# Kernel optimization log

Hardware: AMD Instinct MI355X
Metric: run time of the kernel (lower is better)

## Reference

```python
import jax, jax.numpy as jnp
import numpy as np

B, N, H = 4, 256, 256
BN_EPS = 1e-5
ETA_EPS = 1e-20


def setup_inputs() -> dict:
    key = jax.random.key(0)
    k1, k2, k3, k4 = jax.random.split(key, 4)
    scale = 1.0 / np.sqrt(H)
    return {
        "nodes_features": jax.random.normal(k1, (B, N, H), dtype=jnp.float32),
        "edges_features": jax.random.normal(k2, (B, N, N, H), dtype=jnp.float32),
        "W1": jax.random.normal(k3, (H, H), dtype=jnp.float32) * scale,
        "W2": jax.random.normal(k4, (H, H), dtype=jnp.float32) * scale,
        "gamma": jnp.ones((H,), dtype=jnp.float32),
        "beta": jnp.zeros((H,), dtype=jnp.float32),
    }


def reference(nodes_features, edges_features, W1, W2, gamma, beta):
    # Linear projections (nn.Linear: y = x @ W.T, no bias)
    x_left = jnp.einsum('bnh,oh->bno', nodes_features, W1)       # (B,N,H)
    x_w2 = jnp.einsum('bnh,oh->bno', nodes_features, W2)         # (B,N,H)

    # Edge gating: sigmoid-normalize over neighbor axis j (dim=2)
    sig = jax.nn.sigmoid(edges_features)                         # (B,N,N,H)
    eta = sig / (jnp.sum(sig, axis=2, keepdims=True) + ETA_EPS)  # (B,N,N,H)

    # Weighted aggregation: sum_j eta[b,i,j,h] * x_w2[b,j,h]
    right = jnp.einsum('bijh,bjh->bih', eta, x_w2)               # (B,N,H)

    equ = x_left + right                                         # (B,N,H)

    # BatchNorm1d over channel H with batch stats over (B, N) (training mode,
    # track_running_stats=False -> always uses batch statistics, biased var)
    mean = jnp.mean(equ, axis=(0, 1))                            # (H,)
    var = jnp.var(equ, axis=(0, 1))                              # (H,) biased
    normed = (equ - mean) * jax.lax.rsqrt(var + BN_EPS)
    return normed * gamma + beta
```

## Files before the change

### kernel.cpp

```cpp
#include <hip/hip_runtime.h>
#include <cstddef>

#define BB 4
#define NN 256
#define HH 256
#define BN_EPS 1e-5f
#define ETA_EPS 1e-20f

typedef float f4 __attribute__((ext_vector_type(4)));

__device__ __forceinline__ float fast_sigmoid(float x) {
    float ex = __expf(-x);
    return __builtin_amdgcn_rcpf(1.f + ex);
}

__global__ __launch_bounds__(256) void transpose_kernel(
    const float* __restrict__ W1, const float* __restrict__ W2,
    float* __restrict__ WT1, float* __restrict__ WT2)
{
    const int which = blockIdx.x >> 4;
    const int tile  = blockIdx.x & 15;
    const int tr = (tile >> 2) << 6, tc = (tile & 3) << 6;
    const float* __restrict__ W  = which ? W2 : W1;
    float* __restrict__ WT       = which ? WT2 : WT1;

    __shared__ float tl[64][65];
    const int c = threadIdx.x & 63, p0 = threadIdx.x >> 6;
#pragma unroll
    for (int p = 0; p < 16; ++p) {
        int r = p * 4 + p0;
        tl[c][r] = W[(tr + r) * HH + tc + c];
    }
    __syncthreads();
#pragma unroll
    for (int p = 0; p < 16; ++p) {
        int cc = p * 4 + p0;
        WT[(tc + cc) * HH + tr + c] = tl[cc][c];
    }
}

__global__ __launch_bounds__(256) void proj_kernel(
    const float* __restrict__ nodes, const float* __restrict__ WT1,
    const float* __restrict__ WT2, float* __restrict__ xleft,
    float* __restrict__ xw2)
{
    const int which = blockIdx.x >> 7;
    const int rb    = blockIdx.x & 127;
    const float* __restrict__ WT = which ? WT2 : WT1;
    float* __restrict__ out      = which ? xw2 : xleft;
    const int t = threadIdx.x;

    __shared__ float xs[8][HH];
    {
        f4* xs4 = reinterpret_cast<f4*>(xs);
        const f4* nodes4 = reinterpret_cast<const f4*>(nodes) + rb * 512;
#pragma unroll
        for (int m = 0; m < 2; ++m) xs4[m * 256 + t] = nodes4[m * 256 + t];
    }
    __syncthreads();

    const int oq = t & 63;
    const int hg = t >> 6;
    const f4* __restrict__ WT4 = reinterpret_cast<const f4*>(WT);

    f4 acc[8];
#pragma unroll
    for (int r = 0; r < 8; ++r) acc[r] = (f4){0.f, 0.f, 0.f, 0.f};

    for (int hh = 0; hh < 64; ++hh) {
        const int h = hg * 64 + hh;
        f4 wv = WT4[h * 64 + oq];
#pragma unroll
        for (int r = 0; r < 8; ++r)
            acc[r] += xs[r][h] * wv;
    }

    __shared__ f4 ps[4][8][64];
#pragma unroll
    for (int r = 0; r < 8; ++r) ps[hg][r][oq] = acc[r];
    __syncthreads();

#pragma unroll
    for (int m = 0; m < 2; ++m) {
        int idx = m * 256 + t;
        int r = idx >> 6, o = idx & 63;
        f4 v = ps[0][r][o] + ps[1][r][o] + ps[2][r][o] + ps[3][r][o];
        reinterpret_cast<f4*>(out)[(rb * 8 + r) * 64 + o] = v;
    }
}

__global__ __launch_bounds__(1024) void edge_kernel(
    const float* __restrict__ edges, const float* __restrict__ xw2,
    const float* __restrict__ xleft, float* __restrict__ equ)
{
    const int blk = blockIdx.x;
    const int ig  = blk >> 2;
    const int hs4 = (blk & 3) * 16;
    const int bi0 = ig * 8;
    const int b   = bi0 >> 8;
    const int t   = threadIdx.x;

    __shared__ f4 xw_s[NN][16];

    const f4* __restrict__ xw4 =
        reinterpret_cast<const f4*>(xw2) + (size_t)b * NN * 64;
#pragma unroll
    for (int m = 0; m < 4; ++m) {
        int idx = m * 1024 + t;
        int j = idx >> 4, q = idx & 15;
        xw_s[j][q] = xw4[j * 64 + hs4 + q];
    }
    __syncthreads();

    const int q  = t & 15;
    const int jl = (t >> 4) & 3;
    const int w  = t >> 6;
    const int il = w & 7;
    const int jh = w >> 3;

    const f4* __restrict__ erow =
        reinterpret_cast<const f4*>(edges) +
        ((size_t)(bi0 + il) * NN + jh * 128 + jl) * 64 + hs4 + q;

    float s0[4] = {0.f, 0.f, 0.f, 0.f};
    float s1[4] = {0.f, 0.f, 0.f, 0.f};

#pragma unroll 4
    for (int jj = 0; jj < 32; ++jj) {
        f4 e  = __builtin_nontemporal_load(erow + jj * 256);
        f4 xw = xw_s[jh * 128 + jj * 4 + jl][q];
#pragma unroll
        for (int k = 0; k < 4; ++k) {
            float sg = fast_sigmoid(e[k]);
            s0[k] += sg;
            s1[k] += sg * xw[k];
        }
    }
    __syncthreads();

    float* red = reinterpret_cast<float*>(xw_s);
    {
        const int g = jh * 4 + jl;
        f4* r0 = reinterpret_cast<f4*>(red) + (g * 8 + il) * 16 + q;
        f4* r1 = r0 + 1024;
        *r0 = (f4){s0[0], s0[1], s0[2], s0[3]};
        *r1 = (f4){s1[0], s1[1], s1[2], s1[3]};
    }
    __syncthreads();

    if (t < 512) {
        const int il2 = t >> 6;
        const int ch  = t & 63;
        float S0 = 0.f, S1 = 0.f;
#pragma unroll
        for (int g = 0; g < 8; ++g) {
            S0 += red[(g * 8 + il2) * 64 + ch];
            S1 += red[(g * 8 + il2) * 64 + ch + 4096];
        }
        const size_t off = (size_t)(bi0 + il2) * HH + hs4 * 4 + ch;
        equ[off] = xleft[off] + S1 / (S0 + ETA_EPS);
    }
}

__global__ __launch_bounds__(1024) void stats_kernel(
    const float* __restrict__ equ, const float* __restrict__ gamma,
    const float* __restrict__ beta, float* __restrict__ scale,
    float* __restrict__ shift)
{
    const int t     = threadIdx.x;
    const int ql    = t & 3;
    const int rg    = t >> 2;
    const int qbase = blockIdx.x * 4;

    const f4* __restrict__ equ4 = reinterpret_cast<const f4*>(equ);

    float s[4] = {0.f, 0.f, 0.f, 0.f};
    float qq[4] = {0.f, 0.f, 0.f, 0.f};
    for (int r = rg; r < BB * NN; r += 256) {
        f4 v = equ4[r * 64 + qbase + ql];
#pragma unroll
        for (int k = 0; k < 4; ++k) { s[k] += v[k]; qq[k] += v[k] * v[k]; }
    }

    __shared__ float sp[256][17];
    __shared__ float qp[256][17];
    __shared__ float sp2[16][17];
    __shared__ float qp2[16][17];
#pragma unroll
    for (int k = 0; k < 4; ++k) { sp[rg][ql * 4 + k] = s[k]; qp[rg][ql * 4 + k] = qq[k]; }
    __syncthreads();

    if (t < 256) {
        const int ch = t & 15, seg = t >> 4;
        float S = 0.f, Q = 0.f;
#pragma unroll
        for (int g = 0; g < 16; ++g) { S += sp[seg * 16 + g][ch]; Q += qp[seg * 16 + g][ch]; }
        sp2[seg][ch] = S; qp2[seg][ch] = Q;
    }
    __syncthreads();

    if (t < 16) {
        float S = 0.f, Q = 0.f;
#pragma unroll
        for (int g = 0; g < 16; ++g) { S += sp2[g][t]; Q += qp2[g][t]; }
        const float inv_n = 1.f / (float)(BB * NN);
        float mean = S * inv_n;
        float var  = Q * inv_n - mean * mean;
        float rstd = rsqrtf(var + BN_EPS);
        int cc = blockIdx.x * 16 + t;
        float g  = gamma[cc];
        float bt = beta[cc];
        scale[cc] = rstd * g;
        shift[cc] = bt - mean * rstd * g;
    }
}

__global__ __launch_bounds__(256) void norm_kernel(
    const float* __restrict__ equ, const float* __restrict__ scale,
    const float* __restrict__ shift, float* __restrict__ out)
{
    const int idx = blockIdx.x * 256 + threadIdx.x;
    f4 e  = reinterpret_cast<const f4*>(equ)[idx];
    const int c4 = idx & 63;
    f4 sc = reinterpret_cast<const f4*>(scale)[c4];
    f4 sh = reinterpret_cast<const f4*>(shift)[c4];
    f4 o;
#pragma unroll
    for (int k = 0; k < 4; ++k) o[k] = e[k] * sc[k] + sh[k];
    reinterpret_cast<f4*>(out)[idx] = o;
}

extern "C" void kernel_launch(void* const* d_in, const int* in_sizes, int n_in,
                              void* d_out, int out_size, void* d_ws, size_t ws_size,
                              hipStream_t stream) {
    (void)in_sizes; (void)n_in; (void)out_size; (void)ws_size;

    const float* nodes = (const float*)d_in[0];
    const float* edges = (const float*)d_in[1];
    const float* W1    = (const float*)d_in[2];
    const float* W2    = (const float*)d_in[3];
    const float* gamma = (const float*)d_in[4];
    const float* beta  = (const float*)d_in[5];
    float* out = (float*)d_out;

    const int nBN_H = BB * NN * HH;
    float* ws    = (float*)d_ws;
    float* xleft = ws;
    float* xw2   = ws + nBN_H;
    float* equ   = ws + 2 * nBN_H;
    float* scale = ws + 3 * nBN_H;
    float* shift = ws + 3 * nBN_H + 256;
    float* WT1   = ws + 3 * nBN_H + 512;
    float* WT2   = WT1 + HH * HH;

    transpose_kernel<<<32, 256, 0, stream>>>(W1, W2, WT1, WT2);
    proj_kernel<<<256, 256, 0, stream>>>(nodes, WT1, WT2, xleft, xw2);
    edge_kernel<<<512, 1024, 0, stream>>>(edges, xw2, xleft, equ);
    stats_kernel<<<16, 1024, 0, stream>>>(equ, gamma, beta, scale, shift);
    norm_kernel<<<256, 256, 0, stream>>>(equ, scale, shift, out);
}
```

Baseline: 71.37 us.

## Restructure edge kernel to one row per block and fuse stats with norm

```diff
diff --git a/kernel.cpp b/kernel.cpp
--- a/kernel.cpp
+++ b/kernel.cpp
@@ -89,46 +89,28 @@
     }
 }
 
-__global__ __launch_bounds__(1024) void edge_kernel(
+__global__ __launch_bounds__(512, 6) void edge_kernel(
     const float* __restrict__ edges, const float* __restrict__ xw2,
     const float* __restrict__ xleft, float* __restrict__ equ)
 {
-    const int blk = blockIdx.x;
-    const int ig  = blk >> 2;
-    const int hs4 = (blk & 3) * 16;
-    const int bi0 = ig * 8;
-    const int b   = bi0 >> 8;
-    const int t   = threadIdx.x;
-
-    __shared__ f4 xw_s[NN][16];
-
+    const int bi = blockIdx.x;
+    const int b  = bi >> 8;
+    const int t  = threadIdx.x;
+    const int q  = t & 63;
+    const int jg = t >> 6;
+
+    const f4* __restrict__ e4 =
+        reinterpret_cast<const f4*>(edges) + ((size_t)bi * NN + jg * 32) * 64 + q;
     const f4* __restrict__ xw4 =
-        reinterpret_cast<const f4*>(xw2) + (size_t)b * NN * 64;
-#pragma unroll
-    for (int m = 0; m < 4; ++m) {
-        int idx = m * 1024 + t;
-        int j = idx >> 4, q = idx & 15;
-        xw_s[j][q] = xw4[j * 64 + hs4 + q];
-    }
-    __syncthreads();
-
-    const int q  = t & 15;
-    const int jl = (t >> 4) & 3;
-    const int w  = t >> 6;
-    const int il = w & 7;
-    const int jh = w >> 3;
-
-    const f4* __restrict__ erow =
-        reinterpret_cast<const f4*>(edges) +
-        ((size_t)(bi0 + il) * NN + jh * 128 + jl) * 64 + hs4 + q;
-
-    float s0[4] = {0.f, 0.f, 0.f, 0.f};
-    float s1[4] = {0.f, 0.f, 0.f, 0.f};
-
-#pragma unroll 4
+        reinterpret_cast<const f4*>(xw2) + ((size_t)b * NN + jg * 32) * 64 + q;
+
+    f4 s0 = (f4){0.f, 0.f, 0.f, 0.f};
+    f4 s1 = (f4){0.f, 0.f, 0.f, 0.f};
+
+#pragma unroll 2
     for (int jj = 0; jj < 32; ++jj) {
-        f4 e  = __builtin_nontemporal_load(erow + jj * 256);
-        f4 xw = xw_s[jh * 128 + jj * 4 + jl][q];
+        f4 e  = __builtin_nontemporal_load(e4 + (size_t)jj * 64);
+        f4 xw = xw4[(size_t)jj * 64];
 #pragma unroll
         for (int k = 0; k < 4; ++k) {
             float sg = fast_sigmoid(e[k]);
@@ -136,98 +118,78 @@
             s1[k] += sg * xw[k];
         }
     }
-    __syncthreads();
-
-    float* red = reinterpret_cast<float*>(xw_s);
-    {
-        const int g = jh * 4 + jl;
-        f4* r0 = reinterpret_cast<f4*>(red) + (g * 8 + il) * 16 + q;
-        f4* r1 = r0 + 1024;
-        *r0 = (f4){s0[0], s0[1], s0[2], s0[3]};
-        *r1 = (f4){s1[0], s1[1], s1[2], s1[3]};
-    }
-    __syncthreads();
-
-    if (t < 512) {
-        const int il2 = t >> 6;
-        const int ch  = t & 63;
-        float S0 = 0.f, S1 = 0.f;
-#pragma unroll
-        for (int g = 0; g < 8; ++g) {
-            S0 += red[(g * 8 + il2) * 64 + ch];
-            S1 += red[(g * 8 + il2) * 64 + ch + 4096];
+
+    __shared__ f4 red0[8][64];
+    __shared__ f4 red1[8][64];
+    red0[jg][q] = s0;
+    red1[jg][q] = s1;
+    __syncthreads();
+
+    if (t < 64) {
+        f4 S0 = (f4){0.f, 0.f, 0.f, 0.f};
+        f4 S1 = (f4){0.f, 0.f, 0.f, 0.f};
+#pragma unroll
+        for (int g = 0; g < 8; ++g) { S0 += red0[g][t]; S1 += red1[g][t]; }
+        f4 xl = reinterpret_cast<const f4*>(xleft)[bi * 64 + t];
+        f4 o;
+#pragma unroll
+        for (int k = 0; k < 4; ++k) o[k] = xl[k] + S1[k] / (S0[k] + ETA_EPS);
+        reinterpret_cast<f4*>(equ)[bi * 64 + t] = o;
+    }
+}
+
+__global__ __launch_bounds__(1024) void statsnorm_kernel(
+    const float* __restrict__ equ, const float* __restrict__ gamma,
+    const float* __restrict__ beta, float* __restrict__ out)
+{
+    const int cq = blockIdx.x;
+    const int t  = threadIdx.x;
+    const int lane = t & 63, w = t >> 6;
+
+    f4 v = reinterpret_cast<const f4*>(equ)[t * 64 + cq];
+    f4 s = v;
+    f4 qs = v * v;
+
+#pragma unroll
+    for (int off = 32; off >= 1; off >>= 1) {
+#pragma unroll
+        for (int k = 0; k < 4; ++k) {
+            s[k]  += __shfl_xor(s[k], off);
+            qs[k] += __shfl_xor(qs[k], off);
         }
-        const size_t off = (size_t)(bi0 + il2) * HH + hs4 * 4 + ch;
-        equ[off] = xleft[off] + S1 / (S0 + ETA_EPS);
-    }
-}
-
-__global__ __launch_bounds__(1024) void stats_kernel(
-    const float* __restrict__ equ, const float* __restrict__ gamma,
-    const float* __restrict__ beta, float* __restrict__ scale,
-    float* __restrict__ shift)
-{
-    const int t     = threadIdx.x;
-    const int ql    = t & 3;
-    const int rg    = t >> 2;
-    const int qbase = blockIdx.x * 4;
-
-    const f4* __restrict__ equ4 = reinterpret_cast<const f4*>(equ);
-
-    float s[4] = {0.f, 0.f, 0.f, 0.f};
-    float qq[4] = {0.f, 0.f, 0.f, 0.f};
-    for (int r = rg; r < BB * NN; r += 256) {
-        f4 v = equ4[r * 64 + qbase + ql];
-#pragma unroll
-        for (int k = 0; k < 4; ++k) { s[k] += v[k]; qq[k] += v[k] * v[k]; }
-    }
-
-    __shared__ float sp[256][17];
-    __shared__ float qp[256][17];
-    __shared__ float sp2[16][17];
-    __shared__ float qp2[16][17];
-#pragma unroll
-    for (int k = 0; k < 4; ++k) { sp[rg][ql * 4 + k] = s[k]; qp[rg][ql * 4 + k] = qq[k]; }
-    __syncthreads();
-
-    if (t < 256) {
-        const int ch = t & 15, seg = t >> 4;
-        float S = 0.f, Q = 0.f;
-#pragma unroll
-        for (int g = 0; g < 16; ++g) { S += sp[seg * 16 + g][ch]; Q += qp[seg * 16 + g][ch]; }
-        sp2[seg][ch] = S; qp2[seg][ch] = Q;
-    }
-    __syncthreads();
-
-    if (t < 16) {
-        float S = 0.f, Q = 0.f;
-#pragma unroll
-        for (int g = 0; g < 16; ++g) { S += sp2[g][t]; Q += qp2[g][t]; }
+    }
+
+    __shared__ f4 ws_[16][2];
+    if (lane == 0) { ws_[w][0] = s; ws_[w][1] = qs; }
+    __syncthreads();
+
+    __shared__ f4 sc_s, sh_s;
+    if (t == 0) {
+        f4 S = (f4){0.f, 0.f, 0.f, 0.f};
+        f4 Q = (f4){0.f, 0.f, 0.f, 0.f};
+#pragma unroll
+        for (int g = 0; g < 16; ++g) { S += ws_[g][0]; Q += ws_[g][1]; }
         const float inv_n = 1.f / (float)(BB * NN);
-        float mean = S * inv_n;
-        float var  = Q * inv_n - mean * mean;
-        float rstd = rsqrtf(var + BN_EPS);
-        int cc = blockIdx.x * 16 + t;
-        float g  = gamma[cc];
-        float bt = beta[cc];
-        scale[cc] = rstd * g;
-        shift[cc] = bt - mean * rstd * g;
-    }
-}
-
-__global__ __launch_bounds__(256) void norm_kernel(
-    const float* __restrict__ equ, const float* __restrict__ scale,
-    const float* __restrict__ shift, float* __restrict__ out)
-{
-    const int idx = blockIdx.x * 256 + threadIdx.x;
-    f4 e  = reinterpret_cast<const f4*>(equ)[idx];
-    const int c4 = idx & 63;
-    f4 sc = reinterpret_cast<const f4*>(scale)[c4];
-    f4 sh = reinterpret_cast<const f4*>(shift)[c4];
+        f4 gm = reinterpret_cast<const f4*>(gamma)[cq];
+        f4 bt = reinterpret_cast<const f4*>(beta)[cq];
+        f4 sc, sh;
+#pragma unroll
+        for (int k = 0; k < 4; ++k) {
+            float mean = S[k] * inv_n;
+            float var  = Q[k] * inv_n - mean * mean;
+            float rstd = rsqrtf(var + BN_EPS);
+            sc[k] = rstd * gm[k];
+            sh[k] = bt[k] - mean * rstd * gm[k];
+        }
+        sc_s = sc; sh_s = sh;
+    }
+    __syncthreads();
+
+    f4 sc = sc_s, sh = sh_s;
     f4 o;
 #pragma unroll
-    for (int k = 0; k < 4; ++k) o[k] = e[k] * sc[k] + sh[k];
-    reinterpret_cast<f4*>(out)[idx] = o;
+    for (int k = 0; k < 4; ++k) o[k] = v[k] * sc[k] + sh[k];
+    reinterpret_cast<f4*>(out)[t * 64 + cq] = o;
 }
 
 extern "C" void kernel_launch(void* const* d_in, const int* in_sizes, int n_in,
@@ -248,14 +210,11 @@
     float* xleft = ws;
     float* xw2   = ws + nBN_H;
     float* equ   = ws + 2 * nBN_H;
-    float* scale = ws + 3 * nBN_H;
-    float* shift = ws + 3 * nBN_H + 256;
-    float* WT1   = ws + 3 * nBN_H + 512;
+    float* WT1   = ws + 3 * nBN_H;
     float* WT2   = WT1 + HH * HH;
 
     transpose_kernel<<<32, 256, 0, stream>>>(W1, W2, WT1, WT2);
     proj_kernel<<<256, 256, 0, stream>>>(nodes, WT1, WT2, xleft, xw2);
-    edge_kernel<<<512, 1024, 0, stream>>>(edges, xw2, xleft, equ);
-    stats_kernel<<<16, 1024, 0, stream>>>(equ, gamma, beta, scale, shift);
-    norm_kernel<<<256, 256, 0, stream>>>(equ, scale, shift, out);
-}
+    edge_kernel<<<BB * NN, 512, 0, stream>>>(edges, xw2, xleft, equ);
+    statsnorm_kernel<<<64, 1024, 0, stream>>>(equ, gamma, beta, out);
+}
```

Result: slower. 79.83 us (+11.9%).
